# Kernel tuning notes

Hardware: AMD Instinct MI355X
Metric: run time of the kernel (lower is better)

The kernel has to match this reference:

```python
import jax, jax.numpy as jnp
import numpy as np

QF = 28  # quality_factor from init

_BASE_QUANT = np.array([
    [16, 11, 10, 16, 24, 40, 51, 61],
    [12, 12, 14, 19, 26, 58, 60, 55],
    [14, 13, 16, 24, 40, 57, 69, 56],
    [14, 17, 22, 29, 51, 87, 80, 62],
    [18, 22, 37, 56, 68, 109, 103, 77],
    [24, 35, 55, 64, 81, 104, 113, 92],
    [49, 64, 78, 87, 103, 121, 120, 101],
    [72, 92, 95, 98, 112, 100, 103, 99]], dtype=np.float32)

def _quant_matrix(qf: int) -> jnp.ndarray:
    scale = 50.0 / max(1, qf) if qf < 25 else 200.0 - 2 * qf
    return jnp.asarray(np.maximum(_BASE_QUANT * scale / 50.0, 1.0), dtype=jnp.float32)

def _dct_basis(N: int = 8) -> jnp.ndarray:
    # Orthonormal DCT-II basis: basis @ x @ basis.T is the 2D DCT (norm='ortho')
    k = np.arange(N)[:, None].astype(np.float32)
    n = np.arange(N)[None, :].astype(np.float32)
    b = np.sqrt(2.0 / N) * np.cos(np.pi * k * (2 * n + 1) / (2 * N))
    b[0, :] = np.sqrt(1.0 / N)
    return jnp.asarray(b, dtype=jnp.float32)

def setup_inputs() -> dict:
    key = jax.random.key(0)
    x = jax.random.uniform(key, (8, 3, 1080, 1920), dtype=jnp.float32) * 255.0
    return {"x": x}

def reference(x):
    B, C, H, W = x.shape
    basis = _dct_basis(8)
    q = _quant_matrix(QF)  # (8, 8)

    # BGR -> Y (luminance)
    b, g, r = x[:, 0:1], x[:, 1:2], x[:, 2:3]
    y = 0.114 * b + 0.587 * g + 0.299 * r  # (B, 1, H, W)

    # pad to multiple of 8 (replicate)
    pad_h, pad_w = (-H) % 8, (-W) % 8
    yp = jnp.pad(y, ((0, 0), (0, 0), (0, pad_h), (0, pad_w)), mode='edge') if (pad_h or pad_w) else y
    Hp, Wp = H + pad_h, W + pad_w
    nh, nw = Hp // 8, Wp // 8

    # split into 8x8 blocks: (B, 1, nh, nw, 8, 8)
    blocks = yp.reshape(B, 1, nh, 8, nw, 8).transpose(0, 1, 2, 4, 3, 5)

    # 2D DCT (ortho): basis @ block @ basis.T
    coef = jnp.einsum('ki,...ij,lj->...kl', basis, blocks, basis)

    # hard quantization with straight-through estimator (training-mode forward == hard)
    qhard = jnp.round(coef / (q + 1e-8)) * q
    coef_q = coef + jax.lax.stop_gradient(qhard - coef)

    # 2D inverse DCT: basis.T @ block @ basis
    rec = jnp.einsum('ik,...ij,jl->...kl', basis, coef_q, basis)

    # reassemble blocks -> image, crop padding
    y_rec = rec.transpose(0, 1, 2, 4, 3, 5).reshape(B, 1, Hp, Wp)[:, :, :H, :W]

    # Y back to BGR: add luminance delta weighted by the BGR->Y coefficients
    yd = y_rec - y
    out = jnp.concatenate([b + 0.114 * yd, g + 0.587 * yd, r + 0.299 * yd], axis=1)
    return jnp.clip(out, 0.0, 255.0)
```

## Files before the change

kernel.cpp:

```cpp
#include <hip/hip_runtime.h>
#include <math.h>

#define IMG_H 1080
#define IMG_W 1920
#define HW (IMG_H * IMG_W)
#define NBATCH 8

__device__ __constant__ int BASEQ[64] = {
    16, 11, 10, 16, 24, 40, 51, 61,
    12, 12, 14, 19, 26, 58, 60, 55,
    14, 13, 16, 24, 40, 57, 69, 56,
    14, 17, 22, 29, 51, 87, 80, 62,
    18, 22, 37, 56, 68, 109, 103, 77,
    24, 35, 55, 64, 81, 104, 113, 92,
    49, 64, 78, 87, 103, 121, 120, 101,
    72, 92, 95, 98, 112, 100, 103, 99};

__device__ __forceinline__ float clamp255(float v) {
    return fminf(fmaxf(v, 0.0f), 255.0f);
}

__global__ __launch_bounds__(128) void h264_kernel(const float* __restrict__ x,
                                                   float* __restrict__ out) {
    __shared__ __align__(16) float yt[8 * 128];
    __shared__ float t2[16 * 72];
    __shared__ float bl[64];
    __shared__ float ql[64];

    const int t = threadIdx.x;
    const int w0 = blockIdx.x * 128;
    const int h0 = blockIdx.y * 8;
    const int bat = blockIdx.z;

    if (t < 64) {
        int k = t >> 3, n = t & 7;
        float v;
        if (k == 0) {
            v = 0.35355339059327373f;
        } else {
            float a = 3.14159265358979323846f * (float)k;
            a = a * (2.0f * (float)n + 1.0f);
            a = a / 16.0f;
            v = 0.5f * cosf(a);
        }
        bl[t] = v;
        ql[t] = __fdiv_rn((float)(BASEQ[t] * 144), 50.0f);
    }

    const float* xb = x + (size_t)bat * 3 * HW;
    float* ob = out + (size_t)bat * 3 * HW;

    float4 Bv[2], Gv[2], Rv[2];
    int gaddr[2];
#pragma unroll
    for (int it = 0; it < 2; ++it) {
        int idx = t + 128 * it;
        int row = idx >> 5;
        int c4 = (idx & 31) << 2;
        int ga = (h0 + row) * IMG_W + w0 + c4;
        gaddr[it] = ga;
        Bv[it] = *(const float4*)(xb + ga);
        Gv[it] = *(const float4*)(xb + HW + ga);
        Rv[it] = *(const float4*)(xb + 2 * HW + ga);
        float4 y4;
        y4.x = __fadd_rn(__fadd_rn(__fmul_rn(0.114f, Bv[it].x), __fmul_rn(0.587f, Gv[it].x)), __fmul_rn(0.299f, Rv[it].x));
        y4.y = __fadd_rn(__fadd_rn(__fmul_rn(0.114f, Bv[it].y), __fmul_rn(0.587f, Gv[it].y)), __fmul_rn(0.299f, Rv[it].y));
        y4.z = __fadd_rn(__fadd_rn(__fmul_rn(0.114f, Bv[it].z), __fmul_rn(0.587f, Gv[it].z)), __fmul_rn(0.299f, Rv[it].z));
        y4.w = __fadd_rn(__fadd_rn(__fmul_rn(0.114f, Bv[it].w), __fmul_rn(0.587f, Gv[it].w)), __fmul_rn(0.299f, Rv[it].w));
        *(float4*)(yt + row * 128 + c4) = y4;
    }
    __syncthreads();

    const int blk = t >> 3;
    const int l = t & 7;
    float* t2b = t2 + blk * 72;

    float ycol[8];
#pragma unroll
    for (int i = 0; i < 8; ++i) ycol[i] = yt[i * 128 + t];

    float c1[8];
#pragma unroll
    for (int k = 0; k < 8; ++k) {
        float acc = 0.0f;
#pragma unroll
        for (int i = 0; i < 8; ++i) acc = fmaf(bl[k * 8 + i], ycol[i], acc);
        c1[k] = acc;
    }
#pragma unroll
    for (int k = 0; k < 8; ++k) t2b[l * 9 + k] = c1[k];
    __syncthreads();

    float coef[8];
#pragma unroll
    for (int k = 0; k < 8; ++k) {
        float acc = 0.0f;
#pragma unroll
        for (int j = 0; j < 8; ++j) acc = fmaf(t2b[j * 9 + k], bl[l * 8 + j], acc);
        float q = ql[k * 8 + l];
        coef[k] = __fmul_rn(rintf(__fdiv_rn(acc, q)), q);
    }
    __syncthreads();
#pragma unroll
    for (int k = 0; k < 8; ++k) t2b[l * 9 + k] = coef[k];
    __syncthreads();

    float s[8];
#pragma unroll
    for (int i = 0; i < 8; ++i) {
        float acc = 0.0f;
#pragma unroll
        for (int j = 0; j < 8; ++j) acc = fmaf(t2b[j * 9 + i], bl[j * 8 + l], acc);
        s[i] = acc;
    }
    float yd[8];
#pragma unroll
    for (int k = 0; k < 8; ++k) {
        float acc = 0.0f;
#pragma unroll
        for (int i = 0; i < 8; ++i) acc = fmaf(bl[i * 8 + k], s[i], acc);
        yd[k] = __fsub_rn(acc, ycol[k]);
    }
#pragma unroll
    for (int k = 0; k < 8; ++k) yt[k * 128 + t] = yd[k];
    __syncthreads();

#pragma unroll
    for (int it = 0; it < 2; ++it) {
        int idx = t + 128 * it;
        int row = idx >> 5;
        int c4 = (idx & 31) << 2;
        float4 y4 = *(float4*)(yt + row * 128 + c4);
        int ga = gaddr[it];
        float4 o0, o1, o2;
        o0.x = clamp255(__fadd_rn(Bv[it].x, __fmul_rn(0.114f, y4.x)));
        o0.y = clamp255(__fadd_rn(Bv[it].y, __fmul_rn(0.114f, y4.y)));
        o0.z = clamp255(__fadd_rn(Bv[it].z, __fmul_rn(0.114f, y4.z)));
        o0.w = clamp255(__fadd_rn(Bv[it].w, __fmul_rn(0.114f, y4.w)));
        o1.x = clamp255(__fadd_rn(Gv[it].x, __fmul_rn(0.587f, y4.x)));
        o1.y = clamp255(__fadd_rn(Gv[it].y, __fmul_rn(0.587f, y4.y)));
        o1.z = clamp255(__fadd_rn(Gv[it].z, __fmul_rn(0.587f, y4.z)));
        o1.w = clamp255(__fadd_rn(Gv[it].w, __fmul_rn(0.587f, y4.w)));
        o2.x = clamp255(__fadd_rn(Rv[it].x, __fmul_rn(0.299f, y4.x)));
        o2.y = clamp255(__fadd_rn(Rv[it].y, __fmul_rn(0.299f, y4.y)));
        o2.z = clamp255(__fadd_rn(Rv[it].z, __fmul_rn(0.299f, y4.z)));
        o2.w = clamp255(__fadd_rn(Rv[it].w, __fmul_rn(0.299f, y4.w)));
        *(float4*)(ob + ga) = o0;
        *(float4*)(ob + HW + ga) = o1;
        *(float4*)(ob + 2 * HW + ga) = o2;
    }
}

extern "C" void kernel_launch(void* const* d_in, const int* in_sizes, int n_in,
                              void* d_out, int out_size, void* d_ws, size_t ws_size,
                              hipStream_t stream) {
    const float* x = (const float*)d_in[0];
    float* out = (float*)d_out;
    dim3 grid(IMG_W / 128, IMG_H / 8, NBATCH);
    dim3 block(128);
    h264_kernel<<<grid, block, 0, stream>>>(x, out);
}
```

Measured before the change: 329.4 us.

## Make each wave own a 64-column tile and replace block barriers with wave fences

Restructures the kernel so each 64-lane wave processes its own 8x64 strip in private LDS regions. This lets the workgroup-wide __syncthreads calls become wave-local LDS waitcnt fences. The block grows to 192 threads (three waves, 192 columns), and global loads and stores become nontemporal to avoid cache pollution in this streaming kernel. Wave-level fences depend on wavefront-64 execution. The bl/ql tables are now written redundantly by every wave, and nothing synchronises those writes with reads from other waves.

```diff
diff --git a/kernel.cpp b/kernel.cpp
--- a/kernel.cpp
+++ b/kernel.cpp
@@ -5,6 +5,8 @@
 #define IMG_W 1920
 #define HW (IMG_H * IMG_W)
 #define NBATCH 8
+
+typedef float f4 __attribute__((ext_vector_type(4)));
 
 __device__ __constant__ int BASEQ[64] = {
     16, 11, 10, 16, 24, 40, 51, 61,
@@ -20,20 +22,25 @@
     return fminf(fmaxf(v, 0.0f), 255.0f);
 }
 
-__global__ __launch_bounds__(128) void h264_kernel(const float* __restrict__ x,
+__device__ __forceinline__ void wave_lds_fence() {
+    __builtin_amdgcn_wave_barrier();
+    __builtin_amdgcn_s_waitcnt(0xC07F);
+    __builtin_amdgcn_wave_barrier();
+}
+
+__global__ __launch_bounds__(192) void h264_kernel(const float* __restrict__ x,
                                                    float* __restrict__ out) {
-    __shared__ __align__(16) float yt[8 * 128];
-    __shared__ float t2[16 * 72];
+    __shared__ __align__(16) float yt[3 * 512];
+    __shared__ float t2[3 * 576];
     __shared__ float bl[64];
     __shared__ float ql[64];
 
     const int t = threadIdx.x;
-    const int w0 = blockIdx.x * 128;
-    const int h0 = blockIdx.y * 8;
-    const int bat = blockIdx.z;
+    const int wave = t >> 6;
+    const int lane = t & 63;
 
-    if (t < 64) {
-        int k = t >> 3, n = t & 7;
+    {
+        int k = lane >> 3, n = lane & 7;
         float v;
         if (k == 0) {
             v = 0.35355339059327373f;
@@ -43,41 +50,47 @@
             a = a / 16.0f;
             v = 0.5f * cosf(a);
         }
-        bl[t] = v;
-        ql[t] = __fdiv_rn((float)(BASEQ[t] * 144), 50.0f);
+        bl[lane] = v;
+        ql[lane] = __fdiv_rn((float)(BASEQ[lane] * 144), 50.0f);
     }
 
+    const int h0 = blockIdx.y * 8;
+    const int wcol0 = blockIdx.x * 192 + wave * 64;
+    const int bat = blockIdx.z;
     const float* xb = x + (size_t)bat * 3 * HW;
     float* ob = out + (size_t)bat * 3 * HW;
 
-    float4 Bv[2], Gv[2], Rv[2];
+    float* ytw = yt + wave * 512;
+    float* t2w = t2 + wave * 576;
+
+    f4 Bv[2], Gv[2], Rv[2];
     int gaddr[2];
 #pragma unroll
     for (int it = 0; it < 2; ++it) {
-        int idx = t + 128 * it;
-        int row = idx >> 5;
-        int c4 = (idx & 31) << 2;
-        int ga = (h0 + row) * IMG_W + w0 + c4;
+        int idx = lane + (it << 6);
+        int row = idx >> 4;
+        int c4 = (idx & 15) << 2;
+        int ga = (h0 + row) * IMG_W + wcol0 + c4;
         gaddr[it] = ga;
-        Bv[it] = *(const float4*)(xb + ga);
-        Gv[it] = *(const float4*)(xb + HW + ga);
-        Rv[it] = *(const float4*)(xb + 2 * HW + ga);
-        float4 y4;
+        Bv[it] = __builtin_nontemporal_load((const f4*)(xb + ga));
+        Gv[it] = __builtin_nontemporal_load((const f4*)(xb + HW + ga));
+        Rv[it] = __builtin_nontemporal_load((const f4*)(xb + 2 * HW + ga));
+        f4 y4;
         y4.x = __fadd_rn(__fadd_rn(__fmul_rn(0.114f, Bv[it].x), __fmul_rn(0.587f, Gv[it].x)), __fmul_rn(0.299f, Rv[it].x));
         y4.y = __fadd_rn(__fadd_rn(__fmul_rn(0.114f, Bv[it].y), __fmul_rn(0.587f, Gv[it].y)), __fmul_rn(0.299f, Rv[it].y));
         y4.z = __fadd_rn(__fadd_rn(__fmul_rn(0.114f, Bv[it].z), __fmul_rn(0.587f, Gv[it].z)), __fmul_rn(0.299f, Rv[it].z));
         y4.w = __fadd_rn(__fadd_rn(__fmul_rn(0.114f, Bv[it].w), __fmul_rn(0.587f, Gv[it].w)), __fmul_rn(0.299f, Rv[it].w));
-        *(float4*)(yt + row * 128 + c4) = y4;
+        *(f4*)(ytw + row * 64 + c4) = y4;
     }
-    __syncthreads();
+    wave_lds_fence();
 
-    const int blk = t >> 3;
-    const int l = t & 7;
-    float* t2b = t2 + blk * 72;
+    const int blk = lane >> 3;
+    const int l = lane & 7;
+    float* t2b = t2w + blk * 72;
 
     float ycol[8];
 #pragma unroll
-    for (int i = 0; i < 8; ++i) ycol[i] = yt[i * 128 + t];
+    for (int i = 0; i < 8; ++i) ycol[i] = ytw[i * 64 + lane];
 
     float c1[8];
 #pragma unroll
@@ -89,7 +102,7 @@
     }
 #pragma unroll
     for (int k = 0; k < 8; ++k) t2b[l * 9 + k] = c1[k];
-    __syncthreads();
+    wave_lds_fence();
 
     float coef[8];
 #pragma unroll
@@ -100,10 +113,10 @@
         float q = ql[k * 8 + l];
         coef[k] = __fmul_rn(rintf(__fdiv_rn(acc, q)), q);
     }
-    __syncthreads();
+    wave_lds_fence();
 #pragma unroll
     for (int k = 0; k < 8; ++k) t2b[l * 9 + k] = coef[k];
-    __syncthreads();
+    wave_lds_fence();
 
     float s[8];
 #pragma unroll
@@ -122,17 +135,17 @@
         yd[k] = __fsub_rn(acc, ycol[k]);
     }
 #pragma unroll
-    for (int k = 0; k < 8; ++k) yt[k * 128 + t] = yd[k];
-    __syncthreads();
+    for (int k = 0; k < 8; ++k) ytw[k * 64 + lane] = yd[k];
+    wave_lds_fence();
 
 #pragma unroll
     for (int it = 0; it < 2; ++it) {
-        int idx = t + 128 * it;
-        int row = idx >> 5;
-        int c4 = (idx & 31) << 2;
-        float4 y4 = *(float4*)(yt + row * 128 + c4);
+        int idx = lane + (it << 6);
+        int row = idx >> 4;
+        int c4 = (idx & 15) << 2;
+        f4 y4 = *(f4*)(ytw + row * 64 + c4);
         int ga = gaddr[it];
-        float4 o0, o1, o2;
+        f4 o0, o1, o2;
         o0.x = clamp255(__fadd_rn(Bv[it].x, __fmul_rn(0.114f, y4.x)));
         o0.y = clamp255(__fadd_rn(Bv[it].y, __fmul_rn(0.114f, y4.y)));
         o0.z = clamp255(__fadd_rn(Bv[it].z, __fmul_rn(0.114f, y4.z)));
@@ -145,9 +158,9 @@
         o2.y = clamp255(__fadd_rn(Rv[it].y, __fmul_rn(0.299f, y4.y)));
         o2.z = clamp255(__fadd_rn(Rv[it].z, __fmul_rn(0.299f, y4.z)));
         o2.w = clamp255(__fadd_rn(Rv[it].w, __fmul_rn(0.299f, y4.w)));
-        *(float4*)(ob + ga) = o0;
-        *(float4*)(ob + HW + ga) = o1;
-        *(float4*)(ob + 2 * HW + ga) = o2;
+        __builtin_nontemporal_store(o0, (f4*)(ob + ga));
+        __builtin_nontemporal_store(o1, (f4*)(ob + HW + ga));
+        __builtin_nontemporal_store(o2, (f4*)(ob + 2 * HW + ga));
     }
 }
 
@@ -156,7 +169,7 @@
                               hipStream_t stream) {
     const float* x = (const float*)d_in[0];
     float* out = (float*)d_out;
-    dim3 grid(IMG_W / 128, IMG_H / 8, NBATCH);
-    dim3 block(128);
+    dim3 grid(IMG_W / 192, IMG_H / 8, NBATCH);
+    dim3 block(192);
     h264_kernel<<<grid, block, 0, stream>>>(x, out);
 }
```

Measured after the change: 316.0 us. 4.1% less time.
